# Optimization experiments

Hardware: AMD Instinct MI355X
Metric: run time of the kernel (lower is better)

Reference implementation:

```python
import jax, jax.numpy as jnp
import numpy as np

H, C, PQ, PV = 12, 16, 4, 8   # heads, c_hidden, qk points, v points
CS, CZ = 384, 128
INF, EPS = 1e5, 1e-8


def quat_to_rot(q):
    w, x, y, z = q[..., 0], q[..., 1], q[..., 2], q[..., 3]
    r = jnp.stack([
        1 - 2 * (y * y + z * z), 2 * (x * y - w * z), 2 * (x * z + w * y),
        2 * (x * y + w * z), 1 - 2 * (x * x + z * z), 2 * (y * z - w * x),
        2 * (x * z - w * y), 2 * (y * z + w * x), 1 - 2 * (x * x + y * y)],
        axis=-1)
    return r.reshape(q.shape[:-1] + (3, 3))


def setup_inputs() -> dict:
    key = jax.random.key(0)
    ks = jax.random.split(key, 20)
    B, N = 1, 768
    s = jax.random.normal(ks[0], (B, N, CS), jnp.float32)
    z = jax.random.normal(ks[1], (B, N, N, CZ), jnp.float32)
    quat = jax.random.normal(ks[2], (B, N, 4), jnp.float32)
    quat = quat / jnp.linalg.norm(quat, axis=-1, keepdims=True)
    rot = quat_to_rot(quat)
    trans = 10.0 * jax.random.normal(ks[3], (B, N, 3), jnp.float32)
    mask = jnp.ones((B, N), jnp.float32)
    ss = jax.random.uniform(ks[4], (B, N, N), jnp.float32)
    sc = 0.02
    W_q = sc * jax.random.normal(ks[5], (CS, H * C), jnp.float32)
    b_q = jnp.zeros((H * C,), jnp.float32)
    W_kv = sc * jax.random.normal(ks[6], (CS, 2 * H * C), jnp.float32)
    b_kv = jnp.zeros((2 * H * C,), jnp.float32)
    W_qp = sc * jax.random.normal(ks[7], (CS, H * PQ * 3), jnp.float32)
    b_qp = jnp.zeros((H * PQ * 3,), jnp.float32)
    W_kvp = sc * jax.random.normal(ks[8], (CS, H * (PQ + PV) * 3), jnp.float32)
    b_kvp = jnp.zeros((H * (PQ + PV) * 3,), jnp.float32)
    W_b = sc * jax.random.normal(ks[9], (CZ, H), jnp.float32)
    b_b = jnp.zeros((H,), jnp.float32)
    head_weights = 0.1 * jax.random.normal(ks[10], (H,), jnp.float32)
    cdim = H * (CZ + C + PV * 4)
    W_out = sc * jax.random.normal(ks[11], (cdim, CS), jnp.float32)
    b_out = jnp.zeros((CS,), jnp.float32)
    return dict(s=s, z=z, rot=rot, trans=trans, mask=mask, ss=ss,
                W_q=W_q, b_q=b_q, W_kv=W_kv, b_kv=b_kv, W_qp=W_qp, b_qp=b_qp,
                W_kvp=W_kvp, b_kvp=b_kvp, W_b=W_b, b_b=b_b,
                head_weights=head_weights, W_out=W_out, b_out=b_out)


def reference(s, z, rot, trans, mask, ss, W_q, b_q, W_kv, b_kv, W_qp, b_qp,
              W_kvp, b_kvp, W_b, b_b, head_weights, W_out, b_out):
    B, N, _ = s.shape
    # scalar q/k/v  [B,N,H,C]
    q = (s @ W_q + b_q).reshape(B, N, H, C)
    kv = (s @ W_kv + b_kv).reshape(B, N, H, 2 * C)
    k, v = kv[..., :C], kv[..., C:]
    # point q/k/v: linear output is [x_all, y_all, z_all] -> stack on last dim
    qp = s @ W_qp + b_qp                                  # [B,N,H*PQ*3]
    qp = jnp.stack(jnp.split(qp, 3, axis=-1), axis=-1)    # [B,N,H*PQ,3] local
    qp = jnp.einsum('bnxy,bnpy->bnpx', rot, qp) + trans[:, :, None]
    qp = qp.reshape(B, N, H, PQ, 3)                       # global frame
    kvp = s @ W_kvp + b_kvp
    kvp = jnp.stack(jnp.split(kvp, 3, axis=-1), axis=-1)  # [B,N,H*(PQ+PV),3]
    kvp = jnp.einsum('bnxy,bnpy->bnpx', rot, kvp) + trans[:, :, None]
    kvp = kvp.reshape(B, N, H, PQ + PV, 3)
    kp, vp = kvp[..., :PQ, :], kvp[..., PQ:, :]
    # scalar attention logits + pair bias
    b = z @ W_b + b_b                                     # [B,N,N,H]
    a = jnp.einsum('bihc,bjhc->bhij', q, k) * np.sqrt(1.0 / (3 * C))
    a = a + np.sqrt(1.0 / 3) * jnp.transpose(b, (0, 3, 1, 2))
    # point-distance attention
    diff = qp[:, :, None] - kp[:, None]                   # [B,N,N,H,PQ,3]
    d2 = jnp.sum(diff * diff, axis=-1)                    # [B,N,N,H,PQ]
    hw = jax.nn.softplus(head_weights) * np.sqrt(1.0 / (3 * (PQ * 9.0 / 2)))
    pt = -0.5 * jnp.sum(d2 * hw[None, None, None, :, None], axis=-1)  # [B,N,N,H]
    a = a + jnp.transpose(pt, (0, 3, 1, 2))
    sq_mask = INF * (mask[:, :, None] * mask[:, None, :] - 1.0)
    a = a + sq_mask[:, None]
    # weighted softmax (ss_usage='multiply', t_ss=1): weights = exp(ss) - 0.99
    weights = jnp.exp(ss) - 0.99                          # [B,N,N]
    e = jnp.exp(a - jnp.max(a, axis=-1, keepdims=True))
    we = e * weights[:, None]
    a = we / jnp.sum(we, axis=-1, keepdims=True)          # [B,H,N,N]
    # outputs
    o = jnp.einsum('bhij,bjhc->bihc', a, v).reshape(B, N, H * C)
    o_pt = jnp.einsum('bhij,bjhpc->bihpc', a, vp)         # [B,N,H,PV,3] global
    o_pt = jnp.einsum('bnyx,bnhpy->bnhpx', rot, o_pt - trans[:, :, None, None])
    o_pt_norm = jnp.sqrt(jnp.sum(o_pt ** 2, axis=-1) + EPS).reshape(B, N, H * PV)
    o_pt = o_pt.reshape(B, N, H * PV, 3)
    o_pair = jnp.einsum('bhij,bijc->bihc', a, z).reshape(B, N, H * CZ)
    cat = jnp.concatenate(
        [o, o_pt[..., 0], o_pt[..., 1], o_pt[..., 2], o_pt_norm, o_pair], axis=-1)
    return cat @ W_out + b_out
```

## Files before the change

kernel.cpp:

```cpp
#include <hip/hip_runtime.h>
#include <math.h>

#define NN 768
#define CSD 384
#define HD 12
#define CD 16
#define PQD 4
#define PVD 8
#define CZD 128
#define CATD 2112

#define OFF_Q      0u
#define OFF_K      147456u
#define OFF_V      294912u
#define OFF_QP     442368u
#define OFF_KP     552960u
#define OFF_VP     663552u
#define OFF_RAW    884736u
#define OFF_B      1327104u
#define OFF_A      8404992u
#define OFF_CAT    15482880u

__device__ __forceinline__ float wcol_val(const float* Wq, const float* Wkv,
                                          const float* Wqp, const float* Wkvp,
                                          int k, int col) {
  if (col < 192) return Wq[k*192 + col];
  if (col < 576) return Wkv[k*384 + (col-192)];
  if (col < 720) return Wqp[k*144 + (col-576)];
  return Wkvp[k*432 + (col-720)];
}
__device__ __forceinline__ float bias_val(const float* bq, const float* bkv,
                                          const float* bqp, const float* bkvp, int col) {
  if (col < 192) return bq[col];
  if (col < 576) return bkv[col-192];
  if (col < 720) return bqp[col-576];
  return bkvp[col-720];
}

__global__ __launch_bounds__(256) void k_proj(const float* __restrict__ s,
    const float* __restrict__ Wq, const float* __restrict__ bq,
    const float* __restrict__ Wkv, const float* __restrict__ bkv,
    const float* __restrict__ Wqp, const float* __restrict__ bqp,
    const float* __restrict__ Wkvp, const float* __restrict__ bkvp,
    float* __restrict__ ws) {
  __shared__ float At[64*17];
  __shared__ float Bt[16*64];
  int t = threadIdx.x;
  int c0 = blockIdx.x * 64;
  int r0 = blockIdx.y * 64;
  float acc[4][4] = {};
  int cc = t & 15, rr = t >> 4;
  for (int kt = 0; kt < CSD; kt += 16) {
    int ka = t & 15, mb = t >> 4;
#pragma unroll
    for (int p = 0; p < 4; ++p) {
      int m = mb + p*16;
      At[m*17 + ka] = s[(r0+m)*CSD + kt + ka];
    }
    int cb = t & 63, kb = t >> 6;
#pragma unroll
    for (int p = 0; p < 4; ++p) {
      int kk = kb + p*4;
      Bt[kk*64 + cb] = wcol_val(Wq,Wkv,Wqp,Wkvp, kt+kk, c0+cb);
    }
    __syncthreads();
#pragma unroll
    for (int k = 0; k < 16; ++k) {
      float a0 = At[(rr*4+0)*17 + k];
      float a1 = At[(rr*4+1)*17 + k];
      float a2 = At[(rr*4+2)*17 + k];
      float a3 = At[(rr*4+3)*17 + k];
      float4 b4 = *(const float4*)&Bt[k*64 + cc*4];
      acc[0][0] = fmaf(a0,b4.x,acc[0][0]); acc[0][1] = fmaf(a0,b4.y,acc[0][1]);
      acc[0][2] = fmaf(a0,b4.z,acc[0][2]); acc[0][3] = fmaf(a0,b4.w,acc[0][3]);
      acc[1][0] = fmaf(a1,b4.x,acc[1][0]); acc[1][1] = fmaf(a1,b4.y,acc[1][1]);
      acc[1][2] = fmaf(a1,b4.z,acc[1][2]); acc[1][3] = fmaf(a1,b4.w,acc[1][3]);
      acc[2][0] = fmaf(a2,b4.x,acc[2][0]); acc[2][1] = fmaf(a2,b4.y,acc[2][1]);
      acc[2][2] = fmaf(a2,b4.z,acc[2][2]); acc[2][3] = fmaf(a2,b4.w,acc[2][3]);
      acc[3][0] = fmaf(a3,b4.x,acc[3][0]); acc[3][1] = fmaf(a3,b4.y,acc[3][1]);
      acc[3][2] = fmaf(a3,b4.z,acc[3][2]); acc[3][3] = fmaf(a3,b4.w,acc[3][3]);
    }
    __syncthreads();
  }
  float* qbuf = ws + OFF_Q; float* kbuf = ws + OFF_K; float* vbuf = ws + OFF_V;
  float* raw  = ws + OFF_RAW;
#pragma unroll
  for (int jj = 0; jj < 4; ++jj) {
    int col = c0 + cc*4 + jj;
    float bv = bias_val(bq,bkv,bqp,bkvp,col);
#pragma unroll
    for (int ii = 0; ii < 4; ++ii) {
      int row = r0 + rr*4 + ii;
      float val = acc[ii][jj] + bv;
      if (col < 192) {
        int h = col >> 4, c = col & 15;
        qbuf[(h*NN + row)*CD + c] = val;
      } else if (col < 576) {
        int u = col - 192; int h = u >> 5; int c2 = u & 31;
        if (c2 < 16) kbuf[(h*NN+row)*CD + c2] = val;
        else         vbuf[(h*NN+row)*CD + (c2-16)] = val;
      } else {
        raw[row*576 + (col-576)] = val;
      }
    }
  }
}

__global__ __launch_bounds__(256) void k_points(const float* __restrict__ rot,
    const float* __restrict__ trans, float* __restrict__ ws) {
  int tg = blockIdx.x*256 + threadIdx.x;
  int n = tg / 192, pidx = tg % 192;
  const float* raw = ws + OFF_RAW + n*576;
  float v0, v1, v2;
  if (pidx < 48) { v0 = raw[pidx]; v1 = raw[48+pidx]; v2 = raw[96+pidx]; }
  else { int pp = pidx-48; v0 = raw[144+pp]; v1 = raw[288+pp]; v2 = raw[432+pp]; }
  const float* R = rot + n*9; const float* T = trans + n*3;
  float g0 = R[0]*v0 + R[1]*v1 + R[2]*v2 + T[0];
  float g1 = R[3]*v0 + R[4]*v1 + R[5]*v2 + T[1];
  float g2 = R[6]*v0 + R[7]*v1 + R[8]*v2 + T[2];
  if (pidx < 48) {
    int h = pidx >> 2, p = pidx & 3;
    float* qp = ws + OFF_QP + ((h*NN + n)*PQD + p)*3;
    qp[0]=g0; qp[1]=g1; qp[2]=g2;
  } else {
    int pp = pidx - 48; int h = pp/12; int q12 = pp - 12*h;
    if (q12 < 4) { float* kp = ws + OFF_KP + ((h*NN+n)*PQD + q12)*3; kp[0]=g0; kp[1]=g1; kp[2]=g2; }
    else         { float* vp = ws + OFF_VP + ((h*NN+n)*PVD + (q12-4))*3; vp[0]=g0; vp[1]=g1; vp[2]=g2; }
  }
}

__global__ __launch_bounds__(256) void k_bias(const float* __restrict__ z,
    const float* __restrict__ Wb, const float* __restrict__ bb, float* __restrict__ ws) {
  int t = threadIdx.x;
  int q = t & 15, g = t >> 4;
  float wbr[8][12];
#pragma unroll
  for (int cc = 0; cc < 8; ++cc) {
    const float* wp = Wb + (q*8 + cc)*HD;
#pragma unroll
    for (int h = 0; h < 12; ++h) wbr[cc][h] = wp[h];
  }
  float bbr[12];
#pragma unroll
  for (int h = 0; h < 12; ++h) bbr[h] = bb[h];

  const int base = blockIdx.x * 512;
  const float* zq = z + (size_t)(base + g)*CZD + q*8;
  float4 p0a = *(const float4*)(zq);
  float4 p0b = *(const float4*)(zq + 4);
  float4 p1a = *(const float4*)(zq + 16*CZD);
  float4 p1b = *(const float4*)(zq + 16*CZD + 4);
  float* bmat = ws + OFF_B;
  const float s2 = 0.57735026918962576f;
  for (int s = 0; s < 32; ++s) {
    float4 za = p0a, zb = p0b;
    p0a = p1a; p0b = p1b;
    if (s < 30) {
      p1a = *(const float4*)(zq + (size_t)(s+2)*16*CZD);
      p1b = *(const float4*)(zq + (size_t)(s+2)*16*CZD + 4);
    }
    float acc[12];
#pragma unroll
    for (int h = 0; h < 12; ++h) acc[h] = 0.f;
#pragma unroll
    for (int h = 0; h < 12; ++h) {
      acc[h] = fmaf(za.x, wbr[0][h], acc[h]);
      acc[h] = fmaf(za.y, wbr[1][h], acc[h]);
      acc[h] = fmaf(za.z, wbr[2][h], acc[h]);
      acc[h] = fmaf(za.w, wbr[3][h], acc[h]);
      acc[h] = fmaf(zb.x, wbr[4][h], acc[h]);
      acc[h] = fmaf(zb.y, wbr[5][h], acc[h]);
      acc[h] = fmaf(zb.z, wbr[6][h], acc[h]);
      acc[h] = fmaf(zb.w, wbr[7][h], acc[h]);
    }
#pragma unroll
    for (int off = 8; off >= 1; off >>= 1)
#pragma unroll
      for (int h = 0; h < 12; ++h) acc[h] += __shfl_xor(acc[h], off);
    if (q == 0) {
      int r = base + g + 16*s;
      int i = r / NN;
      int j = r - i*NN;
#pragma unroll
      for (int h = 0; h < 12; ++h)
        bmat[((size_t)i*HD + h)*NN + j] = s2*(acc[h] + bbr[h]);
    }
  }
}

__global__ __launch_bounds__(256) void k_attn(
    const float* __restrict__ mask, const float* __restrict__ ss,
    const float* __restrict__ hwts, float* __restrict__ ws) {
  int h = blockIdx.x, i = blockIdx.y;
  int t = threadIdx.x;
  __shared__ float qsm[16];
  __shared__ float qpsm[12];
  __shared__ float wred[8];
  const float* qbuf = ws + OFF_Q; const float* kbuf = ws + OFF_K;
  const float* qp   = ws + OFF_QP; const float* kp  = ws + OFF_KP;
  const float* bmat = ws + OFF_B;
  float* abuf = ws + OFF_A;
  if (t < 16) qsm[t] = qbuf[(h*NN+i)*CD + t];
  else if (t < 28) qpsm[t-16] = qp[(h*NN+i)*12 + (t-16)];
  __syncthreads();
  float coef = -0.5f * 0.13608276348795434f * log1pf(__expf(hwts[h]));
  float mi = mask[i];
  const float s1 = 0.14433756729740643f;
  float l3[3], ss3[3];
#pragma unroll
  for (int jj = 0; jj < 3; ++jj) {
    int j = t + jj*256;
    const float4* kb = (const float4*)(kbuf + (h*NN+j)*CD);
    float dot = 0.f;
#pragma unroll
    for (int u = 0; u < 4; ++u) {
      float4 kv = kb[u];
      dot = fmaf(qsm[u*4+0], kv.x, dot);
      dot = fmaf(qsm[u*4+1], kv.y, dot);
      dot = fmaf(qsm[u*4+2], kv.z, dot);
      dot = fmaf(qsm[u*4+3], kv.w, dot);
    }
    const float4* kpb = (const float4*)(kp + (h*NN+j)*12);
    float pts = 0.f;
#pragma unroll
    for (int u = 0; u < 3; ++u) {
      float4 kpv = kpb[u];
      float d;
      d = qpsm[u*4+0]-kpv.x; pts = fmaf(d,d,pts);
      d = qpsm[u*4+1]-kpv.y; pts = fmaf(d,d,pts);
      d = qpsm[u*4+2]-kpv.z; pts = fmaf(d,d,pts);
      d = qpsm[u*4+3]-kpv.w; pts = fmaf(d,d,pts);
    }
    float bterm = bmat[((size_t)i*HD + h)*NN + j];
    float lg = fmaf(dot, s1, bterm) + coef*pts + 100000.0f*(mi*mask[j] - 1.0f);
    l3[jj] = lg; ss3[jj] = ss[i*NN + j];
  }
  float mx = fmaxf(l3[0], fmaxf(l3[1], l3[2]));
#pragma unroll
  for (int off = 32; off >= 1; off >>= 1) mx = fmaxf(mx, __shfl_xor(mx, off));
  if ((t & 63) == 0) wred[t>>6] = mx;
  __syncthreads();
  mx = fmaxf(fmaxf(wred[0],wred[1]), fmaxf(wred[2],wred[3]));
  float e3[3]; float sum = 0.f;
#pragma unroll
  for (int jj = 0; jj < 3; ++jj) {
    e3[jj] = __expf(l3[jj]-mx) * (__expf(ss3[jj]) - 0.99f);
    sum += e3[jj];
  }
#pragma unroll
  for (int off = 32; off >= 1; off >>= 1) sum += __shfl_xor(sum, off);
  if ((t & 63) == 0) wred[4 + (t>>6)] = sum;
  __syncthreads();
  sum = (wred[4]+wred[5]) + (wred[6]+wred[7]);
  float inv = 1.0f / sum;
#pragma unroll
  for (int jj = 0; jj < 3; ++jj)
    abuf[((size_t)h*NN + i)*NN + t + jj*256] = e3[jj]*inv;
}

__global__ __launch_bounds__(256) void k_out_v(
    const float* __restrict__ rot, const float* __restrict__ trans, float* __restrict__ ws) {
  int h = blockIdx.x;
  int i = blockIdx.y*4 + (threadIdx.x >> 6);
  int lane = threadIdx.x & 63;
  const float* abuf = ws + OFF_A; const float* vbuf = ws + OFF_V; const float* vpbuf = ws + OFF_VP;
  float* cat = ws + OFF_CAT;
  const float* arow = abuf + ((size_t)h*NN + i)*NN;
  float acc = 0.f;
  if (lane < 40) {
    const float* ptr; int stride;
    if (lane < 16) { ptr = vbuf + (size_t)(h*NN)*CD + lane; stride = CD; }
    else           { ptr = vpbuf + (size_t)(h*NN)*24 + (lane-16); stride = 24; }
    for (int j = 0; j < NN; j += 4) {
      float4 a4 = *(const float4*)(arow + j);
      float x0 = ptr[0];
      float x1 = ptr[stride];
      float x2 = ptr[2*stride];
      float x3 = ptr[3*stride];
      ptr += 4*stride;
      acc = fmaf(a4.x, x0, acc);
      acc = fmaf(a4.y, x1, acc);
      acc = fmaf(a4.z, x2, acc);
      acc = fmaf(a4.w, x3, acc);
    }
  }
  if (lane < 16) {
    cat[(size_t)i*CATD + h*CD + lane] = acc;
  } else if (lane < 40) {
    int pv = lane - 16; int p = pv/3; int x = pv - 3*p;
    int base = 16 + p*3;
    float g0 = __shfl(acc, base+0);
    float g1 = __shfl(acc, base+1);
    float g2 = __shfl(acc, base+2);
    float v0 = g0 - trans[i*3+0];
    float v1 = g1 - trans[i*3+1];
    float v2 = g2 - trans[i*3+2];
    float loc = rot[i*9 + 0*3 + x]*v0 + rot[i*9 + 1*3 + x]*v1 + rot[i*9 + 2*3 + x]*v2;
    cat[(size_t)i*CATD + 192 + x*96 + h*PVD + p] = loc;
    float sq = loc*loc;
    float n2 = __shfl(sq, base+0) + __shfl(sq, base+1) + __shfl(sq, base+2);
    if (x == 0) cat[(size_t)i*CATD + 480 + h*PVD + p] = sqrtf(n2 + 1e-8f);
  }
}

__global__ __launch_bounds__(256) void k_out_pair(const float* __restrict__ z, float* __restrict__ ws) {
  __shared__ float a_sm[HD*NN];
  __shared__ float4 psm[4][HD][32];
  int i = blockIdx.x;
  int t = threadIdx.x;
  const float* abuf = ws + OFF_A;
  float* cat = ws + OFF_CAT;
  for (int h = 0; h < HD; ++h) {
    if (t < 192)
      *(float4*)&a_sm[h*NN + t*4] = *(const float4*)(abuf + ((size_t)h*NN + i)*NN + t*4);
  }
  __syncthreads();
  int c4 = t & 31, jc = t >> 5;
  const float* zbase = z + ((size_t)i*NN + (size_t)jc*96)*CZD + c4*4;
  float4 acc[12];
#pragma unroll
  for (int h = 0; h < 12; ++h) acc[h] = make_float4(0.f,0.f,0.f,0.f);
  for (int jj = 0; jj < 96; jj += 4) {
    float4 z0 = *(const float4*)(zbase + (size_t)(jj+0)*CZD);
    float4 z1 = *(const float4*)(zbase + (size_t)(jj+1)*CZD);
    float4 z2 = *(const float4*)(zbase + (size_t)(jj+2)*CZD);
    float4 z3 = *(const float4*)(zbase + (size_t)(jj+3)*CZD);
    int j0 = jc*96 + jj;
#pragma unroll
    for (int h = 0; h < 12; ++h) {
      float4 av = *(const float4*)&a_sm[h*NN + j0];
      acc[h].x = fmaf(av.x, z0.x, acc[h].x); acc[h].y = fmaf(av.x, z0.y, acc[h].y);
      acc[h].z = fmaf(av.x, z0.z, acc[h].z); acc[h].w = fmaf(av.x, z0.w, acc[h].w);
      acc[h].x = fmaf(av.y, z1.x, acc[h].x); acc[h].y = fmaf(av.y, z1.y, acc[h].y);
      acc[h].z = fmaf(av.y, z1.z, acc[h].z); acc[h].w = fmaf(av.y, z1.w, acc[h].w);
      acc[h].x = fmaf(av.z, z2.x, acc[h].x); acc[h].y = fmaf(av.z, z2.y, acc[h].y);
      acc[h].z = fmaf(av.z, z2.z, acc[h].z); acc[h].w = fmaf(av.z, z2.w, acc[h].w);
      acc[h].x = fmaf(av.w, z3.x, acc[h].x); acc[h].y = fmaf(av.w, z3.y, acc[h].y);
      acc[h].z = fmaf(av.w, z3.z, acc[h].z); acc[h].w = fmaf(av.w, z3.w, acc[h].w);
    }
  }
  int wv = t >> 6, ln = t & 63;
#pragma unroll
  for (int h = 0; h < 12; ++h) {
    acc[h].x += __shfl_down(acc[h].x, 32);
    acc[h].y += __shfl_down(acc[h].y, 32);
    acc[h].z += __shfl_down(acc[h].z, 32);
    acc[h].w += __shfl_down(acc[h].w, 32);
  }
  if (ln < 32) {
#pragma unroll
    for (int h = 0; h < 12; ++h) psm[wv][h][ln] = acc[h];
  }
  __syncthreads();
  for (int o = t; o < 384; o += 256) {
    int h = o >> 5, cc = o & 31;
    float4 s0 = psm[0][h][cc], s1 = psm[1][h][cc], s2 = psm[2][h][cc], s3 = psm[3][h][cc];
    float4 r;
    r.x = (s0.x+s1.x)+(s2.x+s3.x);
    r.y = (s0.y+s1.y)+(s2.y+s3.y);
    r.z = (s0.z+s1.z)+(s2.z+s3.z);
    r.w = (s0.w+s1.w)+(s2.w+s3.w);
    *(float4*)&cat[(size_t)i*CATD + 576 + h*CZD + cc*4] = r;
  }
}

__global__ __launch_bounds__(256) void k_init_out(const float* __restrict__ bout, float* __restrict__ out) {
  int idx = blockIdx.x*256 + threadIdx.x;
  if (idx < NN*CSD) out[idx] = bout[idx % CSD];
}

__global__ __launch_bounds__(256) void k_final(const float* __restrict__ Wout,
    float* __restrict__ out, const float* __restrict__ ws) {
  __shared__ float At[64*17];
  __shared__ float Bt[16*64];
  const float* cat = ws + OFF_CAT;
  int t = threadIdx.x;
  int c0 = blockIdx.x*64, r0 = blockIdx.y*64;
  int kstart = blockIdx.z*528;
  float acc[4][4] = {};
  int cc = t & 15, rr = t >> 4;
  for (int kt = 0; kt < 528; kt += 16) {
    int ka = t & 15, mb = t >> 4;
#pragma unroll
    for (int p = 0; p < 4; ++p) {
      int m = mb + p*16;
      At[m*17 + ka] = cat[(size_t)(r0+m)*CATD + kstart + kt + ka];
    }
    int cb = t & 63, kb = t >> 6;
#pragma unroll
    for (int p = 0; p < 4; ++p) {
      int kk = kb + p*4;
      Bt[kk*64 + cb] = Wout[(size_t)(kstart+kt+kk)*CSD + c0 + cb];
    }
    __syncthreads();
#pragma unroll
    for (int k = 0; k < 16; ++k) {
      float a0 = At[(rr*4+0)*17 + k];
      float a1 = At[(rr*4+1)*17 + k];
      float a2 = At[(rr*4+2)*17 + k];
      float a3 = At[(rr*4+3)*17 + k];
      float4 b4 = *(const float4*)&Bt[k*64 + cc*4];
      acc[0][0] = fmaf(a0,b4.x,acc[0][0]); acc[0][1] = fmaf(a0,b4.y,acc[0][1]);
      acc[0][2] = fmaf(a0,b4.z,acc[0][2]); acc[0][3] = fmaf(a0,b4.w,acc[0][3]);
      acc[1][0] = fmaf(a1,b4.x,acc[1][0]); acc[1][1] = fmaf(a1,b4.y,acc[1][1]);
      acc[1][2] = fmaf(a1,b4.z,acc[1][2]); acc[1][3] = fmaf(a1,b4.w,acc[1][3]);
      acc[2][0] = fmaf(a2,b4.x,acc[2][0]); acc[2][1] = fmaf(a2,b4.y,acc[2][1]);
      acc[2][2] = fmaf(a2,b4.z,acc[2][2]); acc[2][3] = fmaf(a2,b4.w,acc[2][3]);
      acc[3][0] = fmaf(a3,b4.x,acc[3][0]); acc[3][1] = fmaf(a3,b4.y,acc[3][1]);
      acc[3][2] = fmaf(a3,b4.z,acc[3][2]); acc[3][3] = fmaf(a3,b4.w,acc[3][3]);
    }
    __syncthreads();
  }
#pragma unroll
  for (int ii = 0; ii < 4; ++ii)
#pragma unroll
    for (int jj = 0; jj < 4; ++jj)
      atomicAdd(&out[(size_t)(r0+rr*4+ii)*CSD + c0 + cc*4 + jj], acc[ii][jj]);
}

extern "C" void kernel_launch(void* const* d_in, const int* in_sizes, int n_in,
                              void* d_out, int out_size, void* d_ws, size_t ws_size,
                              hipStream_t stream) {
  const float* s    = (const float*)d_in[0];
  const float* z    = (const float*)d_in[1];
  const float* rot  = (const float*)d_in[2];
  const float* trans= (const float*)d_in[3];
  const float* mask = (const float*)d_in[4];
  const float* ss   = (const float*)d_in[5];
  const float* Wq   = (const float*)d_in[6];
  const float* bq   = (const float*)d_in[7];
  const float* Wkv  = (const float*)d_in[8];
  const float* bkv  = (const float*)d_in[9];
  const float* Wqp  = (const float*)d_in[10];
  const float* bqp  = (const float*)d_in[11];
  const float* Wkvp = (const float*)d_in[12];
  const float* bkvp = (const float*)d_in[13];
  const float* Wb   = (const float*)d_in[14];
  const float* bb   = (const float*)d_in[15];
  const float* hw   = (const float*)d_in[16];
  const float* Wout = (const float*)d_in[17];
  const float* bout = (const float*)d_in[18];
  float* ws  = (float*)d_ws;
  float* out = (float*)d_out;

  hipLaunchKernelGGL(k_proj, dim3(18,12), dim3(256), 0, stream,
                     s, Wq,bq, Wkv,bkv, Wqp,bqp, Wkvp,bkvp, ws);
  hipLaunchKernelGGL(k_points, dim3(576), dim3(256), 0, stream, rot, trans, ws);
  hipLaunchKernelGGL(k_bias, dim3(1152), dim3(256), 0, stream, z, Wb, bb, ws);
  hipLaunchKernelGGL(k_attn, dim3(12,768), dim3(256), 0, stream, mask, ss, hw, ws);
  hipLaunchKernelGGL(k_out_v, dim3(12,192), dim3(256), 0, stream, rot, trans, ws);
  hipLaunchKernelGGL(k_out_pair, dim3(768), dim3(256), 0, stream, z, ws);
  hipLaunchKernelGGL(k_init_out, dim3(1152), dim3(256), 0, stream, bout, out);
  hipLaunchKernelGGL(k_final, dim3(6,12,4), dim3(256), 0, stream, Wout, out, ws);
}
```

Baseline: 849.2 us.

## Stage z tiles in LDS for pair bias, fuse output init, trim pair reduction

The pair-bias kernel now stages 128-row tiles of z through padded shared memory with coalesced loads. It replaces the full 12-head butterfly shuffle reduction with a recursive-halving reduction, so each lane ends up owning one head and writes it directly. The output-bias initialization is folded into extra blocks of the points kernel to save a launch. The pair-output reduction also goes from four partial buffers to two. Together these aim to cut shuffle count and launch overhead, at the cost of more LDS traffic and barriers in the bias kernel.

```diff
diff --git a/kernel.cpp b/kernel.cpp
--- a/kernel.cpp
+++ b/kernel.cpp
@@ -107,8 +107,15 @@
 }
 
 __global__ __launch_bounds__(256) void k_points(const float* __restrict__ rot,
-    const float* __restrict__ trans, float* __restrict__ ws) {
-  int tg = blockIdx.x*256 + threadIdx.x;
+    const float* __restrict__ trans, const float* __restrict__ bout,
+    float* __restrict__ out, float* __restrict__ ws) {
+  int bx = blockIdx.x;
+  if (bx >= 576) {
+    int idx = (bx - 576)*256 + threadIdx.x;
+    out[idx] = bout[idx % CSD];
+    return;
+  }
+  int tg = bx*256 + threadIdx.x;
   int n = tg / 192, pidx = tg % 192;
   const float* raw = ws + OFF_RAW + n*576;
   float v0, v1, v2;
@@ -129,10 +136,14 @@
   }
 }
 
+#define BR 128
+#define BPAD 130
 __global__ __launch_bounds__(256) void k_bias(const float* __restrict__ z,
     const float* __restrict__ Wb, const float* __restrict__ bb, float* __restrict__ ws) {
+  __shared__ float zt[BR*BPAD];
   int t = threadIdx.x;
-  int q = t & 15, g = t >> 4;
+  int q = t & 15;
+  int rg = t >> 4;
   float wbr[8][12];
 #pragma unroll
   for (int cc = 0; cc < 8; ++cc) {
@@ -140,51 +151,79 @@
 #pragma unroll
     for (int h = 0; h < 12; ++h) wbr[cc][h] = wp[h];
   }
-  float bbr[12];
-#pragma unroll
-  for (int h = 0; h < 12; ++h) bbr[h] = bb[h];
-
-  const int base = blockIdx.x * 512;
-  const float* zq = z + (size_t)(base + g)*CZD + q*8;
-  float4 p0a = *(const float4*)(zq);
-  float4 p0b = *(const float4*)(zq + 4);
-  float4 p1a = *(const float4*)(zq + 16*CZD);
-  float4 p1b = *(const float4*)(zq + 16*CZD + 4);
+  const int b3=(q>>3)&1, b2=(q>>2)&1, b1=(q>>1)&1, b0=q&1;
+  const int hmine = 6*b3 + 3*b2 + (b1 ? 2 : b0);
+  const bool writer = !(b1 && b0);
+  const float bbh = bb[hmine];
+
+  const int rowbase = blockIdx.x * 1152;
   float* bmat = ws + OFF_B;
   const float s2 = 0.57735026918962576f;
-  for (int s = 0; s < 32; ++s) {
-    float4 za = p0a, zb = p0b;
-    p0a = p1a; p0b = p1b;
-    if (s < 30) {
-      p1a = *(const float4*)(zq + (size_t)(s+2)*16*CZD);
-      p1b = *(const float4*)(zq + (size_t)(s+2)*16*CZD + 4);
-    }
-    float acc[12];
-#pragma unroll
-    for (int h = 0; h < 12; ++h) acc[h] = 0.f;
-#pragma unroll
-    for (int h = 0; h < 12; ++h) {
-      acc[h] = fmaf(za.x, wbr[0][h], acc[h]);
-      acc[h] = fmaf(za.y, wbr[1][h], acc[h]);
-      acc[h] = fmaf(za.z, wbr[2][h], acc[h]);
-      acc[h] = fmaf(za.w, wbr[3][h], acc[h]);
-      acc[h] = fmaf(zb.x, wbr[4][h], acc[h]);
-      acc[h] = fmaf(zb.y, wbr[5][h], acc[h]);
-      acc[h] = fmaf(zb.z, wbr[6][h], acc[h]);
-      acc[h] = fmaf(zb.w, wbr[7][h], acc[h]);
-    }
-#pragma unroll
-    for (int off = 8; off >= 1; off >>= 1)
-#pragma unroll
-      for (int h = 0; h < 12; ++h) acc[h] += __shfl_xor(acc[h], off);
-    if (q == 0) {
-      int r = base + g + 16*s;
-      int i = r / NN;
-      int j = r - i*NN;
-#pragma unroll
-      for (int h = 0; h < 12; ++h)
-        bmat[((size_t)i*HD + h)*NN + j] = s2*(acc[h] + bbr[h]);
-    }
+
+  for (int T = 0; T < 9; ++T) {
+    int r0 = rowbase + T*BR;
+#pragma unroll 4
+    for (int it = 0; it < 16; ++it) {
+      int g = it*256 + t;
+      int row = g >> 5, f4 = g & 31;
+      float4 v = *(const float4*)(z + (size_t)(r0+row)*CZD + f4*4);
+      float* d = &zt[row*BPAD + f4*4];
+      *(float2*)(d)   = make_float2(v.x, v.y);
+      *(float2*)(d+2) = make_float2(v.z, v.w);
+    }
+    __syncthreads();
+#pragma unroll 2
+    for (int ps = 0; ps < 8; ++ps) {
+      int row = ps*16 + rg;
+      const float* zr = &zt[row*BPAD + q*8];
+      float2 z01 = *(const float2*)(zr);
+      float2 z23 = *(const float2*)(zr+2);
+      float2 z45 = *(const float2*)(zr+4);
+      float2 z67 = *(const float2*)(zr+6);
+      float acc[12];
+#pragma unroll
+      for (int h = 0; h < 12; ++h) {
+        float a = z01.x*wbr[0][h];
+        a = fmaf(z01.y, wbr[1][h], a);
+        a = fmaf(z23.x, wbr[2][h], a);
+        a = fmaf(z23.y, wbr[3][h], a);
+        a = fmaf(z45.x, wbr[4][h], a);
+        a = fmaf(z45.y, wbr[5][h], a);
+        a = fmaf(z67.x, wbr[6][h], a);
+        a = fmaf(z67.y, wbr[7][h], a);
+        acc[h] = a;
+      }
+      float na[6];
+#pragma unroll
+      for (int m = 0; m < 6; ++m) {
+        float keep = b3 ? acc[m+6] : acc[m];
+        float give = b3 ? acc[m]   : acc[m+6];
+        na[m] = keep + __shfl_xor(give, 8);
+      }
+      float nb[3];
+#pragma unroll
+      for (int m = 0; m < 3; ++m) {
+        float keep = b2 ? na[m+3] : na[m];
+        float give = b2 ? na[m]   : na[m+3];
+        nb[m] = keep + __shfl_xor(give, 4);
+      }
+      float k0 = b1 ? nb[2] : nb[0];
+      float g0v = b1 ? nb[0] : nb[2];
+      float k1 = b1 ? 0.f   : nb[1];
+      float g1v = b1 ? nb[1] : 0.f;
+      float c0v = k0 + __shfl_xor(g0v, 2);
+      float c1v = k1 + __shfl_xor(g1v, 2);
+      float k2 = b1 ? c0v : (b0 ? c1v : c0v);
+      float g2v = b1 ? c0v : (b0 ? c0v : c1v);
+      float d0 = k2 + __shfl_xor(g2v, 1);
+      if (writer) {
+        int r = r0 + row;
+        int i = r / NN;
+        int j = r - i*NN;
+        bmat[((size_t)i*HD + hmine)*NN + j] = s2*(d0 + bbh);
+      }
+    }
+    __syncthreads();
   }
 }
 
@@ -305,7 +344,7 @@
 
 __global__ __launch_bounds__(256) void k_out_pair(const float* __restrict__ z, float* __restrict__ ws) {
   __shared__ float a_sm[HD*NN];
-  __shared__ float4 psm[4][HD][32];
+  __shared__ float4 psm[2][HD][32];
   int i = blockIdx.x;
   int t = threadIdx.x;
   const float* abuf = ws + OFF_A;
@@ -347,26 +386,30 @@
     acc[h].z += __shfl_down(acc[h].z, 32);
     acc[h].w += __shfl_down(acc[h].w, 32);
   }
-  if (ln < 32) {
-#pragma unroll
-    for (int h = 0; h < 12; ++h) psm[wv][h][ln] = acc[h];
+  if (wv >= 2 && ln < 32) {
+#pragma unroll
+    for (int h = 0; h < 12; ++h) psm[wv-2][h][ln] = acc[h];
+  }
+  __syncthreads();
+  if (wv < 2 && ln < 32) {
+#pragma unroll
+    for (int h = 0; h < 12; ++h) {
+      float4 p = psm[wv][h][ln];
+      acc[h].x += p.x; acc[h].y += p.y; acc[h].z += p.z; acc[h].w += p.w;
+      psm[wv][h][ln] = acc[h];
+    }
   }
   __syncthreads();
   for (int o = t; o < 384; o += 256) {
     int h = o >> 5, cc = o & 31;
-    float4 s0 = psm[0][h][cc], s1 = psm[1][h][cc], s2 = psm[2][h][cc], s3 = psm[3][h][cc];
+    float4 s0 = psm[0][h][cc], s1 = psm[1][h][cc];
     float4 r;
-    r.x = (s0.x+s1.x)+(s2.x+s3.x);
-    r.y = (s0.y+s1.y)+(s2.y+s3.y);
-    r.z = (s0.z+s1.z)+(s2.z+s3.z);
-    r.w = (s0.w+s1.w)+(s2.w+s3.w);
+    r.x = s0.x + s1.x;
+    r.y = s0.y + s1.y;
+    r.z = s0.z + s1.z;
+    r.w = s0.w + s1.w;
     *(float4*)&cat[(size_t)i*CATD + 576 + h*CZD + cc*4] = r;
   }
-}
-
-__global__ __launch_bounds__(256) void k_init_out(const float* __restrict__ bout, float* __restrict__ out) {
-  int idx = blockIdx.x*256 + threadIdx.x;
-  if (idx < NN*CSD) out[idx] = bout[idx % CSD];
 }
 
 __global__ __launch_bounds__(256) void k_final(const float* __restrict__ Wout,
@@ -445,11 +488,10 @@
 
   hipLaunchKernelGGL(k_proj, dim3(18,12), dim3(256), 0, stream,
                      s, Wq,bq, Wkv,bkv, Wqp,bqp, Wkvp,bkvp, ws);
-  hipLaunchKernelGGL(k_points, dim3(576), dim3(256), 0, stream, rot, trans, ws);
-  hipLaunchKernelGGL(k_bias, dim3(1152), dim3(256), 0, stream, z, Wb, bb, ws);
+  hipLaunchKernelGGL(k_points, dim3(1728), dim3(256), 0, stream, rot, trans, bout, out, ws);
+  hipLaunchKernelGGL(k_bias, dim3(512), dim3(256), 0, stream, z, Wb, bb, ws);
   hipLaunchKernelGGL(k_attn, dim3(12,768), dim3(256), 0, stream, mask, ss, hw, ws);
   hipLaunchKernelGGL(k_out_v, dim3(12,192), dim3(256), 0, stream, rot, trans, ws);
   hipLaunchKernelGGL(k_out_pair, dim3(768), dim3(256), 0, stream, z, ws);
-  hipLaunchKernelGGL(k_init_out, dim3(1152), dim3(256), 0, stream, bout, out);
   hipLaunchKernelGGL(k_final, dim3(6,12,4), dim3(256), 0, stream, Wout, out, ws);
 }
```

Measured after the change: 825.1 us. 2.8% less time.
